# Optimization experiments

Hardware: AMD Instinct MI355X
Metric: run time of the kernel (lower is better)

Reference implementation:

```python
import jax, jax.numpy as jnp
import numpy as np

B = 8192      # batch (num nodes)
D = 256       # embedding dim
K = 8         # positives per node -> nnz = B*K
EPS = 1e-8


def setup_inputs() -> dict:
    key = jax.random.key(0)
    k_emb, k_val = jax.random.split(key)
    embeddings = jax.random.normal(k_emb, (B, D), dtype=jnp.float32)
    # structured sparse positive mask: node i is positive with (i+1..i+K) mod B
    # -> unique pairs, row-major sorted (coalesced), no self loops
    rows = jnp.repeat(jnp.arange(B, dtype=jnp.int64), K)           # [B*K]
    offs = jnp.tile(jnp.arange(1, K + 1, dtype=jnp.int64), B)      # [B*K]
    cols = (rows + offs) % B
    pos_vals = jax.random.uniform(k_val, (B * K,), dtype=jnp.float32)
    temperature = jnp.float32(0.5)  # learnable scalar nn.Parameter
    return {
        "embeddings": embeddings,
        "pos_vals": pos_vals,
        "temperature": temperature,
        "pos_row": rows,
        "pos_col": cols,
    }


def reference(embeddings, pos_vals, temperature, pos_row, pos_col):
    n = embeddings.shape[0]
    # F.normalize(p=2, dim=1) with eps=1e-12
    norm = jnp.linalg.norm(embeddings, axis=1, keepdims=True)
    z = embeddings / jnp.maximum(norm, 1e-12)

    temp = jax.nn.softplus(temperature)
    sim = jnp.matmul(z, z.T) / temp                                 # [B,B]
    sim = sim - jax.lax.stop_gradient(jnp.max(sim, axis=1, keepdims=True))

    pos_dense = jnp.zeros((n, n), dtype=bool).at[pos_row, pos_col].set(True)
    identity = jnp.eye(n, dtype=bool)
    neg_mask = (~pos_dense) & (~identity)

    # pos weights: 'inverse_sim' -> 1 - values, min-max normalized
    pos_w = 1.0 - pos_vals
    pos_w = (pos_w - jnp.min(pos_w)) / (jnp.max(pos_w) - jnp.min(pos_w) + EPS)

    # neg weights: 'inverse_sim' -> min-max over negative sims, +1; weight_mat=1 elsewhere
    neg_min = jnp.min(jnp.where(neg_mask, sim, jnp.inf))
    neg_max = jnp.max(jnp.where(neg_mask, sim, -jnp.inf))
    neg_w = (sim - neg_min) / (neg_max - neg_min + EPS) + 1.0
    log_weight = jnp.where(neg_mask, jnp.log(neg_w), 0.0)

    log_probs = sim - jax.nn.logsumexp(sim + log_weight, axis=1, keepdims=True)

    pos_log = log_probs[pos_row, pos_col]   # same ordering as torch boolean index (coalesced mask)
    loss = -jnp.mean(pos_log * pos_w)
    return loss
```

## Files before the change

kernel.cpp:

```cpp
#include <hip/hip_runtime.h>

#define NB 8192
#define ND 256
#define NMASK 8191
#define CEPS 1e-8f
#define L2E 1.4426950408889634f
#define LN2 0.6931471805599453f
#define SC1 0x7F7F7F7F

#if __has_builtin(__builtin_amdgcn_exp2f)
#define EXP2(x) __builtin_amdgcn_exp2f(x)
#else
#define EXP2(x) exp2f(x)
#endif

#define DPPF(x, ctrl) \
  __int_as_float(__builtin_amdgcn_update_dpp(0, __float_as_int(x), (ctrl), 0xF, 0xF, true))

__device__ __forceinline__ float sum16(float x) {
  x += DPPF(x, 0xB1);
  x += DPPF(x, 0x4E);
  x += DPPF(x, 0x124);
  x += DPPF(x, 0x128);
  return x;
}
__device__ __forceinline__ float min16(float x) {
  x = fminf(x, DPPF(x, 0xB1));
  x = fminf(x, DPPF(x, 0x4E));
  x = fminf(x, DPPF(x, 0x124));
  x = fminf(x, DPPF(x, 0x128));
  return x;
}
__device__ __forceinline__ float max16(float x) {
  x = fmaxf(x, DPPF(x, 0xB1));
  x = fmaxf(x, DPPF(x, 0x4E));
  x = fmaxf(x, DPPF(x, 0x124));
  x = fmaxf(x, DPPF(x, 0x128));
  return x;
}

typedef float f32x4 __attribute__((ext_vector_type(4)));
typedef float f32x2 __attribute__((ext_vector_type(2)));
typedef int v8i __attribute__((ext_vector_type(8)));
typedef int v4i __attribute__((ext_vector_type(4)));
union V8 { v8i v; v4i q[2]; };


__global__ void k_norm(const float* __restrict__ emb, const float* __restrict__ temperature,
                       const float* __restrict__ pos_vals, char* __restrict__ zb8,
                       float* __restrict__ EpF,
                       float* __restrict__ bpvmin, float* __restrict__ bpvmax,
                       float* __restrict__ out) {
  const int tid = threadIdx.x, lane = tid & 63, w = tid >> 6;
  const int bid = blockIdx.x;
  if (bid == 0 && tid == 0) out[0] = 0.f;
  float sp = log1pf(expf(temperature[0]));
  float alpha = sqrtf(L2E / sp);
  int row = bid * 4 + w;
  const float4 e = *(const float4*)(emb + row * ND + lane * 4);
  float ss = e.x * e.x + e.y * e.y + e.z * e.z + e.w * e.w;
#pragma unroll
  for (int mk = 1; mk < 64; mk <<= 1) ss += __shfl_xor(ss, mk, 64);
  float rn = alpha / fmaxf(sqrtf(ss), 1e-12f);
  int pk = __builtin_amdgcn_cvt_pk_fp8_f32(e.x * rn, e.y * rn, 0, 0);
  pk = __builtin_amdgcn_cvt_pk_fp8_f32(e.z * rn, e.w * rn, pk, 1);
  *(int*)(zb8 + row * 256 + lane * 4) = pk;
  if (lane < 2) EpF[row * 2 + lane] = 0.f;
  if (w == 0) {
    float v = (lane < 32) ? pos_vals[bid * 32 + lane] : 0.f;
    float mn = (lane < 32) ? v : INFINITY;
    float mx = (lane < 32) ? v : -INFINITY;
#pragma unroll
    for (int mk = 1; mk < 32; mk <<= 1) {
      mn = fminf(mn, __shfl_xor(mn, mk, 64));
      mx = fmaxf(mx, __shfl_xor(mx, mk, 64));
    }
    if (lane == 0) { bpvmin[bid] = mn; bpvmax[bid] = mx; }
  }
}

__global__ __launch_bounds__(256) void k_gemm(
    const char* __restrict__ zb8, float* __restrict__ EpF,
    float* __restrict__ sBand, float* __restrict__ bmin, float* __restrict__ bmax) {
  __shared__ __align__(16) char smem[32768];
  const int tid = threadIdx.x, lane = tid & 63, w = tid >> 6;
  const int l15 = lane & 15, lq = lane >> 4;
  const int bid = blockIdx.x;
  int d, rb;
  if (bid < 2048) { d = bid >> 6; rb = bid & 63; }
  else { d = 32; rb = bid - 2048; }
  const int cb = (rb + d) & 63;
  const int roww = rb * 128 + w * 32;
  const int colbase = cb * 128;

#pragma unroll
  for (int i = 0; i < 8; ++i) {
    int s = w * 8 + i, T = s >> 1, h = s & 1, ct = T >> 1, kc = T & 1;
    const char* g = zb8 + (colbase + ct * 16 + l15) * 256 + kc * 128 + lq * 32 + h * 16;
    __builtin_amdgcn_global_load_lds(
        (const __attribute__((address_space(1))) void*)(g),
        (__attribute__((address_space(3))) void*)(smem + s * 1024), 16, 0, 0);
  }

  V8 aF[2][2];
#pragma unroll
  for (int mt = 0; mt < 2; ++mt) {
    const char* ar = zb8 + (roww + mt * 16 + l15) * 256 + lq * 32;
#pragma unroll
    for (int kc = 0; kc < 2; ++kc) {
      aF[mt][kc].q[0] = *(const v4i*)(ar + kc * 128);
      aF[mt][kc].q[1] = *(const v4i*)(ar + kc * 128 + 16);
    }
  }

  f32x2 E1v[4], Eav[4];
#pragma unroll
  for (int i = 0; i < 4; ++i) { E1v[i] = (f32x2){0.f, 0.f}; Eav[i] = (f32x2){0.f, 0.f}; }
  float2 cA[4][2];
#pragma unroll
  for (int s = 0; s < 4; ++s) { cA[s][0] = make_float2(0.f, 0.f); cA[s][1] = make_float2(0.f, 0.f); }
  float vmn = INFINITY, vmx = -INFINITY;

  __syncthreads();

#pragma unroll
  for (int step = 0; step < 4; ++step) {
    f32x4 acc[2][2];
#pragma unroll
    for (int mt = 0; mt < 2; ++mt) {
      acc[mt][0] = (f32x4){0.f, 0.f, 0.f, 0.f};
      acc[mt][1] = (f32x4){0.f, 0.f, 0.f, 0.f};
    }
#pragma unroll
    for (int kc = 0; kc < 2; ++kc) {
      V8 b0, b1;
      const char* t0 = smem + ((step * 2 + 0) * 2 + kc) * 2048;
      const char* t1 = smem + ((step * 2 + 1) * 2 + kc) * 2048;
      b0.q[0] = *(const v4i*)(t0 + lane * 16);
      b0.q[1] = *(const v4i*)(t0 + 1024 + lane * 16);
      b1.q[0] = *(const v4i*)(t1 + lane * 16);
      b1.q[1] = *(const v4i*)(t1 + 1024 + lane * 16);
#pragma unroll
      for (int mt = 0; mt < 2; ++mt) {
        acc[mt][0] = __builtin_amdgcn_mfma_scale_f32_16x16x128_f8f6f4(
            aF[mt][kc].v, b0.v, acc[mt][0], 0, 0, 0, SC1, 0, SC1);
        acc[mt][1] = __builtin_amdgcn_mfma_scale_f32_16x16x128_f8f6f4(
            aF[mt][kc].v, b1.v, acc[mt][1], 0, 0, 0, SC1, 0, SC1);
      }
    }
    const int offbase = (colbase + step * 32 + l15) - (roww + lq * 4);
    if (d >= 2) {
#pragma unroll
      for (int mt = 0; mt < 2; ++mt)
#pragma unroll
        for (int nt = 0; nt < 2; ++nt) {
          f32x2 t01, t23, e01, e23;
          t01.x = acc[mt][nt][0]; t01.y = acc[mt][nt][1];
          t23.x = acc[mt][nt][2]; t23.y = acc[mt][nt][3];
          e01.x = EXP2(t01.x); e01.y = EXP2(t01.y);
          e23.x = EXP2(t23.x); e23.y = EXP2(t23.y);
          f32x2 m01 = e01 * t01, m23 = e23 * t23;
          E1v[mt * 2 + 0] += e01; E1v[mt * 2 + 1] += e23;
          Eav[mt * 2 + 0] += m01; Eav[mt * 2 + 1] += m23;
          f32x2 es = e01 + e23, ms = m01 + m23;
          cA[step][nt].x += es.x + es.y;
          cA[step][nt].y += ms.x + ms.y;
          vmn = fminf(fminf(t01.x, t01.y), vmn);
          vmn = fminf(fminf(t23.x, t23.y), vmn);
          vmx = fmaxf(fmaxf(t01.x, t01.y), vmx);
          vmx = fmaxf(fmaxf(t23.x, t23.y), vmx);
        }
    } else if (d == 1) {
#pragma unroll
      for (int mt = 0; mt < 2; ++mt)
#pragma unroll
        for (int nt = 0; nt < 2; ++nt)
#pragma unroll
          for (int reg = 0; reg < 4; ++reg) {
            float t = acc[mt][nt][reg];
            float e = EXP2(t);
            E1v[mt * 2 + (reg >> 1)][reg & 1] += e;
            Eav[mt * 2 + (reg >> 1)][reg & 1] = fmaf(e, t, Eav[mt * 2 + (reg >> 1)][reg & 1]);
            cA[step][nt].x += e;
            cA[step][nt].y = fmaf(e, t, cA[step][nt].y);
            vmn = fminf(vmn, t);
            vmx = fmaxf(vmx, t);
            int off = (offbase + (nt - mt) * 16 - reg) & NMASK;
            if (off <= 8)
              sBand[(roww + mt * 16 + lq * 4 + reg) * 16 + off] = t;
          }
    } else {
#pragma unroll
      for (int mt = 0; mt < 2; ++mt)
#pragma unroll
        for (int nt = 0; nt < 2; ++nt)
#pragma unroll
          for (int reg = 0; reg < 4; ++reg) {
            float t = acc[mt][nt][reg];
            float e = EXP2(t);
            E1v[mt * 2 + (reg >> 1)][reg & 1] += e;
            Eav[mt * 2 + (reg >> 1)][reg & 1] = fmaf(e, t, Eav[mt * 2 + (reg >> 1)][reg & 1]);
            int off = (offbase + (nt - mt) * 16 - reg) & NMASK;
            bool isB = off <= 8;
            vmn = fminf(vmn, isB ? vmn : t);
            vmx = fmaxf(vmx, isB ? vmx : t);
            if (isB)
              sBand[(roww + mt * 16 + lq * 4 + reg) * 16 + off] = t;
          }
    }
  }

#pragma unroll
  for (int i = 0; i < 4; ++i) {
    E1v[i].x = sum16(E1v[i].x); E1v[i].y = sum16(E1v[i].y);
    Eav[i].x = sum16(Eav[i].x); Eav[i].y = sum16(Eav[i].y);
  }
  if (l15 == 0) {
#pragma unroll
    for (int mt = 0; mt < 2; ++mt)
#pragma unroll
      for (int p = 0; p < 2; ++p) {
        int r0 = roww + mt * 16 + lq * 4 + p * 2;
        atomicAdd(&EpF[r0 * 2 + 0], E1v[mt * 2 + p].x);
        atomicAdd(&EpF[r0 * 2 + 1], Eav[mt * 2 + p].x);
        atomicAdd(&EpF[r0 * 2 + 2], E1v[mt * 2 + p].y);
        atomicAdd(&EpF[r0 * 2 + 3], Eav[mt * 2 + p].y);
      }
  }
  vmn = min16(vmn);
  vmx = max16(vmx);
  vmn = fminf(vmn, __shfl_xor(vmn, 16, 64));
  vmx = fmaxf(vmx, __shfl_xor(vmx, 16, 64));
  vmn = fminf(vmn, __shfl_xor(vmn, 32, 64));
  vmx = fmaxf(vmx, __shfl_xor(vmx, 32, 64));
  __syncthreads();
  float2* colAcc = (float2*)smem;
  float* redmm = (float*)(smem + 16384);
  if (d != 0) {
#pragma unroll
    for (int s = 0; s < 4; ++s)
#pragma unroll
      for (int nt = 0; nt < 2; ++nt)
        colAcc[(w * 4 + lq) * 128 + s * 32 + nt * 16 + l15] = cA[s][nt];
  }
  if (lane == 0) { redmm[w] = vmn; redmm[4 + w] = vmx; }
  __syncthreads();
  if (d != 0 && tid < 128) {
    float sx = 0.f, sy = 0.f;
#pragma unroll
    for (int j = 0; j < 16; ++j) {
      float2 p = colAcc[j * 128 + tid];
      sx += p.x;
      sy += p.y;
    }
    atomicAdd(&EpF[(colbase + tid) * 2 + 0], sx);
    atomicAdd(&EpF[(colbase + tid) * 2 + 1], sy);
  }
  if (tid == 0) {
    bmin[bid] = fminf(fminf(redmm[0], redmm[1]), fminf(redmm[2], redmm[3]));
    bmax[bid] = fmaxf(fmaxf(redmm[4], redmm[5]), fmaxf(redmm[6], redmm[7]));
  }
}

__global__ void k_final(const float* __restrict__ pos_vals, const float* __restrict__ EpF,
                        const float* __restrict__ sBand,
                        const float* __restrict__ bmin, const float* __restrict__ bmax,
                        const float* __restrict__ bpvmin, const float* __restrict__ bpvmax,
                        float* __restrict__ out) {
  const int tid = threadIdx.x, lane = tid & 63, w = tid >> 6;
  __shared__ float sv[16];
  __shared__ float coef[4];
  float mn = INFINITY, mx = -INFINITY, pmn = INFINITY, pmx = -INFINITY;
  for (int i = tid; i < 2080; i += 256) { mn = fminf(mn, bmin[i]); mx = fmaxf(mx, bmax[i]); }
  for (int i = tid; i < 2048; i += 256) { pmn = fminf(pmn, bpvmin[i]); pmx = fmaxf(pmx, bpvmax[i]); }
#pragma unroll
  for (int mk = 1; mk < 64; mk <<= 1) {
    mn = fminf(mn, __shfl_xor(mn, mk, 64));
    mx = fmaxf(mx, __shfl_xor(mx, mk, 64));
    pmn = fminf(pmn, __shfl_xor(pmn, mk, 64));
    pmx = fmaxf(pmx, __shfl_xor(pmx, mk, 64));
  }
  if (lane == 0) { sv[w] = mn; sv[4 + w] = mx; sv[8 + w] = pmn; sv[12 + w] = pmx; }
  __syncthreads();
  if (tid == 0) {
    float tmin = fminf(fminf(sv[0], sv[1]), fminf(sv[2], sv[3]));
    float tmax = fmaxf(fmaxf(sv[4], sv[5]), fmaxf(sv[6], sv[7]));
    float pvmin = fminf(fminf(sv[8], sv[9]), fminf(sv[10], sv[11]));
    float pvmax = fmaxf(fmaxf(sv[12], sv[13]), fmaxf(sv[14], sv[15]));
    float At = LN2 / ((tmax - tmin) * LN2 + CEPS);
    coef[0] = At;
    coef[1] = 1.f - At * tmin;
    coef[2] = pvmax;
    coef[3] = 1.f / (pvmax - pvmin + CEPS);
  }
  __syncthreads();
  const float At = coef[0], Bt = coef[1], pvmax = coef[2], pwInv = coef[3];

  const int row = blockIdx.x * 256 + tid;
  const float2 ep = *(const float2*)(EpF + row * 2);
  float e1 = ep.x, ea = ep.y;
  const float4* sb4 = (const float4*)(sBand + (size_t)row * 16);
  float4 b0 = sb4[0], b1 = sb4[1], b2 = sb4[2];
  float tb[9] = {b0.x, b0.y, b0.z, b0.w, b1.x, b1.y, b1.z, b1.w, b2.x};
  float Sb = 0.f, Sbt = 0.f;
#pragma unroll
  for (int o = 0; o <= 8; ++o) {
    float e = EXP2(tb[o]);
    Sb += e;
    Sbt = fmaf(e, tb[o], Sbt);
  }
  float denom = At * (ea - Sbt) + Bt * (e1 - Sb) + Sb;
  float lse = logf(denom);
  const float4* pv4 = (const float4*)(pos_vals + (size_t)row * 8);
  float4 pva = pv4[0], pvb = pv4[1];
  float pv[8] = {pva.x, pva.y, pva.z, pva.w, pvb.x, pvb.y, pvb.z, pvb.w};
  float contrib = 0.f;
#pragma unroll
  for (int k = 0; k < 8; ++k)
    contrib += (pvmax - pv[k]) * pwInv * (tb[k + 1] * LN2 - lse);
#pragma unroll
  for (int mk = 1; mk < 64; mk <<= 1) contrib += __shfl_xor(contrib, mk, 64);
  __syncthreads();
  if (lane == 0) sv[w] = contrib;
  __syncthreads();
  if (tid == 0)
    atomicAdd(out, -(sv[0] + sv[1] + sv[2] + sv[3]) * (1.0f / 65536.0f));
}

extern "C" void kernel_launch(void* const* d_in, const int* in_sizes, int n_in,
                              void* d_out, int out_size, void* d_ws, size_t ws_size,
                              hipStream_t stream) {
  const float* emb = (const float*)d_in[0];
  const float* pos_vals = (const float*)d_in[1];
  const float* temperature = (const float*)d_in[2];
  float* out = (float*)d_out;

  char* ws = (char*)d_ws;
  size_t off = 0;
  float* EpF = (float*)(ws + off); off += (size_t)NB * 2 * 4;
  float* sBand = (float*)(ws + off); off += (size_t)NB * 16 * 4;
  float* bmin = (float*)(ws + off); off += 2080 * 4 + 128;
  float* bmax = (float*)(ws + off); off += 2080 * 4 + 128;
  float* bpvmin = (float*)(ws + off); off += 2048 * 4;
  float* bpvmax = (float*)(ws + off); off += 2048 * 4;
  char* zb8 = (char*)(ws + off); off += (size_t)NB * 256;

  k_norm<<<2048, 256, 0, stream>>>(emb, temperature, pos_vals, zb8, EpF, bpvmin, bpvmax, out);
  k_gemm<<<2080, 256, 0, stream>>>(zb8, EpF, sBand, bmin, bmax);
  k_final<<<32, 256, 0, stream>>>(pos_vals, EpF, sBand, bmin, bmax, bpvmin, bpvmax, out);
}
```

Before: 101.0 us.

## Fuse norm, GEMM and final passes into one cooperative persistent kernel

```diff
diff --git a/kernel.cpp b/kernel.cpp
--- a/kernel.cpp
+++ b/kernel.cpp
@@ -1,4 +1,7 @@
 #include <hip/hip_runtime.h>
+#include <hip/hip_cooperative_groups.h>
+
+namespace cg = cooperative_groups;
 
 #define NB 8192
 #define ND 256
@@ -7,6 +10,7 @@
 #define L2E 1.4426950408889634f
 #define LN2 0.6931471805599453f
 #define SC1 0x7F7F7F7F
+#define NTILE 2080
 
 #if __has_builtin(__builtin_amdgcn_exp2f)
 #define EXP2(x) __builtin_amdgcn_exp2f(x)
@@ -45,6 +49,303 @@
 typedef int v4i __attribute__((ext_vector_type(4)));
 union V8 { v8i v; v4i q[2]; };
 
+
+__global__ __launch_bounds__(256) void k_all(
+    const float* __restrict__ emb, const float* __restrict__ pos_vals,
+    const float* __restrict__ temperature, char* __restrict__ zb8,
+    float* __restrict__ EpF, float* __restrict__ sBand,
+    float* __restrict__ bmin, float* __restrict__ bmax,
+    float* __restrict__ bpvmin, float* __restrict__ bpvmax,
+    float* __restrict__ out) {
+  __shared__ __align__(16) char smem[32768];
+  const int tid = threadIdx.x, lane = tid & 63, w = tid >> 6;
+  const int l15 = lane & 15, lq = lane >> 4;
+  const int bid = blockIdx.x, g = gridDim.x;
+  const int gtid = bid * 256 + tid, nth = g * 256;
+  cg::grid_group grid = cg::this_grid();
+
+  {
+    float sp = log1pf(expf(temperature[0]));
+    float alpha = sqrtf(L2E / sp);
+    const int nwave = g * 4, gw = bid * 4 + w;
+    for (int row = gw; row < NB; row += nwave) {
+      const float4 e = *(const float4*)(emb + row * ND + lane * 4);
+      float ss = e.x * e.x + e.y * e.y + e.z * e.z + e.w * e.w;
+#pragma unroll
+      for (int mk = 1; mk < 64; mk <<= 1) ss += __shfl_xor(ss, mk, 64);
+      float rn = alpha / fmaxf(sqrtf(ss), 1e-12f);
+      int pk = __builtin_amdgcn_cvt_pk_fp8_f32(e.x * rn, e.y * rn, 0, 0);
+      pk = __builtin_amdgcn_cvt_pk_fp8_f32(e.z * rn, e.w * rn, pk, 1);
+      *(int*)(zb8 + row * 256 + lane * 4) = pk;
+    }
+    for (int i = gtid; i < NB * 2; i += nth) EpF[i] = 0.f;
+    if (gtid == 0) out[0] = 0.f;
+    float pmn = INFINITY, pmx = -INFINITY;
+    for (int i = gtid; i < NB * 8; i += nth) {
+      float v = pos_vals[i];
+      pmn = fminf(pmn, v);
+      pmx = fmaxf(pmx, v);
+    }
+#pragma unroll
+    for (int mk = 1; mk < 64; mk <<= 1) {
+      pmn = fminf(pmn, __shfl_xor(pmn, mk, 64));
+      pmx = fmaxf(pmx, __shfl_xor(pmx, mk, 64));
+    }
+    float* s0 = (float*)smem;
+    if (lane == 0) { s0[w] = pmn; s0[4 + w] = pmx; }
+    __syncthreads();
+    if (tid == 0) {
+      bpvmin[bid] = fminf(fminf(s0[0], s0[1]), fminf(s0[2], s0[3]));
+      bpvmax[bid] = fmaxf(fmaxf(s0[4], s0[5]), fmaxf(s0[6], s0[7]));
+    }
+  }
+  __threadfence();
+  grid.sync();
+
+  float vmn = INFINITY, vmx = -INFINITY;
+  for (int tile = bid; tile < NTILE; tile += g) {
+    int d, rb;
+    if (tile < 2048) { d = tile >> 6; rb = tile & 63; }
+    else { d = 32; rb = tile - 2048; }
+    const int cb = (rb + d) & 63;
+    const int roww = rb * 128 + w * 32;
+    const int colbase = cb * 128;
+
+    __syncthreads();
+#pragma unroll
+    for (int i = 0; i < 8; ++i) {
+      int s = w * 8 + i, T = s >> 1, h = s & 1, ct = T >> 1, kc = T & 1;
+      const char* gp = zb8 + (colbase + ct * 16 + l15) * 256 + kc * 128 + lq * 32 + h * 16;
+      __builtin_amdgcn_global_load_lds(
+          (const __attribute__((address_space(1))) void*)(gp),
+          (__attribute__((address_space(3))) void*)(smem + s * 1024), 16, 0, 0);
+    }
+    V8 aF[2][2];
+#pragma unroll
+    for (int mt = 0; mt < 2; ++mt) {
+      const char* ar = zb8 + (roww + mt * 16 + l15) * 256 + lq * 32;
+#pragma unroll
+      for (int kc = 0; kc < 2; ++kc) {
+        aF[mt][kc].q[0] = *(const v4i*)(ar + kc * 128);
+        aF[mt][kc].q[1] = *(const v4i*)(ar + kc * 128 + 16);
+      }
+    }
+    f32x2 E1v[4], Eav[4];
+#pragma unroll
+    for (int i = 0; i < 4; ++i) { E1v[i] = (f32x2){0.f, 0.f}; Eav[i] = (f32x2){0.f, 0.f}; }
+    float2 cA[4][2];
+#pragma unroll
+    for (int s = 0; s < 4; ++s) { cA[s][0] = make_float2(0.f, 0.f); cA[s][1] = make_float2(0.f, 0.f); }
+
+    __syncthreads();
+
+#pragma unroll
+    for (int step = 0; step < 4; ++step) {
+      f32x4 acc[2][2];
+#pragma unroll
+      for (int mt = 0; mt < 2; ++mt) {
+        acc[mt][0] = (f32x4){0.f, 0.f, 0.f, 0.f};
+        acc[mt][1] = (f32x4){0.f, 0.f, 0.f, 0.f};
+      }
+#pragma unroll
+      for (int kc = 0; kc < 2; ++kc) {
+        V8 b0, b1;
+        const char* t0 = smem + ((step * 2 + 0) * 2 + kc) * 2048;
+        const char* t1 = smem + ((step * 2 + 1) * 2 + kc) * 2048;
+        b0.q[0] = *(const v4i*)(t0 + lane * 16);
+        b0.q[1] = *(const v4i*)(t0 + 1024 + lane * 16);
+        b1.q[0] = *(const v4i*)(t1 + lane * 16);
+        b1.q[1] = *(const v4i*)(t1 + 1024 + lane * 16);
+#pragma unroll
+        for (int mt = 0; mt < 2; ++mt) {
+          acc[mt][0] = __builtin_amdgcn_mfma_scale_f32_16x16x128_f8f6f4(
+              aF[mt][kc].v, b0.v, acc[mt][0], 0, 0, 0, SC1, 0, SC1);
+          acc[mt][1] = __builtin_amdgcn_mfma_scale_f32_16x16x128_f8f6f4(
+              aF[mt][kc].v, b1.v, acc[mt][1], 0, 0, 0, SC1, 0, SC1);
+        }
+      }
+      const int offbase = (colbase + step * 32 + l15) - (roww + lq * 4);
+      if (d >= 2) {
+#pragma unroll
+        for (int mt = 0; mt < 2; ++mt)
+#pragma unroll
+          for (int nt = 0; nt < 2; ++nt) {
+            f32x2 t01, t23, e01, e23;
+            t01.x = acc[mt][nt][0]; t01.y = acc[mt][nt][1];
+            t23.x = acc[mt][nt][2]; t23.y = acc[mt][nt][3];
+            e01.x = EXP2(t01.x); e01.y = EXP2(t01.y);
+            e23.x = EXP2(t23.x); e23.y = EXP2(t23.y);
+            f32x2 m01 = e01 * t01, m23 = e23 * t23;
+            E1v[mt * 2 + 0] += e01; E1v[mt * 2 + 1] += e23;
+            Eav[mt * 2 + 0] += m01; Eav[mt * 2 + 1] += m23;
+            f32x2 es = e01 + e23, ms = m01 + m23;
+            cA[step][nt].x += es.x + es.y;
+            cA[step][nt].y += ms.x + ms.y;
+            vmn = fminf(fminf(t01.x, t01.y), vmn);
+            vmn = fminf(fminf(t23.x, t23.y), vmn);
+            vmx = fmaxf(fmaxf(t01.x, t01.y), vmx);
+            vmx = fmaxf(fmaxf(t23.x, t23.y), vmx);
+          }
+      } else if (d == 1) {
+#pragma unroll
+        for (int mt = 0; mt < 2; ++mt)
+#pragma unroll
+          for (int nt = 0; nt < 2; ++nt)
+#pragma unroll
+            for (int reg = 0; reg < 4; ++reg) {
+              float t = acc[mt][nt][reg];
+              float e = EXP2(t);
+              E1v[mt * 2 + (reg >> 1)][reg & 1] += e;
+              Eav[mt * 2 + (reg >> 1)][reg & 1] = fmaf(e, t, Eav[mt * 2 + (reg >> 1)][reg & 1]);
+              cA[step][nt].x += e;
+              cA[step][nt].y = fmaf(e, t, cA[step][nt].y);
+              vmn = fminf(vmn, t);
+              vmx = fmaxf(vmx, t);
+              int off = (offbase + (nt - mt) * 16 - reg) & NMASK;
+              if (off <= 8)
+                sBand[(roww + mt * 16 + lq * 4 + reg) * 16 + off] = t;
+            }
+      } else {
+#pragma unroll
+        for (int mt = 0; mt < 2; ++mt)
+#pragma unroll
+          for (int nt = 0; nt < 2; ++nt)
+#pragma unroll
+            for (int reg = 0; reg < 4; ++reg) {
+              float t = acc[mt][nt][reg];
+              float e = EXP2(t);
+              E1v[mt * 2 + (reg >> 1)][reg & 1] += e;
+              Eav[mt * 2 + (reg >> 1)][reg & 1] = fmaf(e, t, Eav[mt * 2 + (reg >> 1)][reg & 1]);
+              int off = (offbase + (nt - mt) * 16 - reg) & NMASK;
+              bool isB = off <= 8;
+              vmn = fminf(vmn, isB ? vmn : t);
+              vmx = fmaxf(vmx, isB ? vmx : t);
+              if (isB)
+                sBand[(roww + mt * 16 + lq * 4 + reg) * 16 + off] = t;
+            }
+      }
+    }
+
+#pragma unroll
+    for (int i = 0; i < 4; ++i) {
+      E1v[i].x = sum16(E1v[i].x); E1v[i].y = sum16(E1v[i].y);
+      Eav[i].x = sum16(Eav[i].x); Eav[i].y = sum16(Eav[i].y);
+    }
+    if (l15 == 0) {
+#pragma unroll
+      for (int mt = 0; mt < 2; ++mt)
+#pragma unroll
+        for (int p = 0; p < 2; ++p) {
+          int r0 = roww + mt * 16 + lq * 4 + p * 2;
+          atomicAdd(&EpF[r0 * 2 + 0], E1v[mt * 2 + p].x);
+          atomicAdd(&EpF[r0 * 2 + 1], Eav[mt * 2 + p].x);
+          atomicAdd(&EpF[r0 * 2 + 2], E1v[mt * 2 + p].y);
+          atomicAdd(&EpF[r0 * 2 + 3], Eav[mt * 2 + p].y);
+        }
+    }
+    __syncthreads();
+    float2* colAcc = (float2*)smem;
+    if (d != 0) {
+#pragma unroll
+      for (int s = 0; s < 4; ++s)
+#pragma unroll
+        for (int nt = 0; nt < 2; ++nt)
+          colAcc[(w * 4 + lq) * 128 + s * 32 + nt * 16 + l15] = cA[s][nt];
+    }
+    __syncthreads();
+    if (d != 0 && tid < 128) {
+      float sx = 0.f, sy = 0.f;
+#pragma unroll
+      for (int j = 0; j < 16; ++j) {
+        float2 p = colAcc[j * 128 + tid];
+        sx += p.x;
+        sy += p.y;
+      }
+      atomicAdd(&EpF[(colbase + tid) * 2 + 0], sx);
+      atomicAdd(&EpF[(colbase + tid) * 2 + 1], sy);
+    }
+  }
+  vmn = min16(vmn);
+  vmx = max16(vmx);
+  vmn = fminf(vmn, __shfl_xor(vmn, 16, 64));
+  vmx = fmaxf(vmx, __shfl_xor(vmx, 16, 64));
+  vmn = fminf(vmn, __shfl_xor(vmn, 32, 64));
+  vmx = fmaxf(vmx, __shfl_xor(vmx, 32, 64));
+  __syncthreads();
+  float* redmm = (float*)(smem + 16384);
+  if (lane == 0) { redmm[w] = vmn; redmm[4 + w] = vmx; }
+  __syncthreads();
+  if (tid == 0) {
+    bmin[bid] = fminf(fminf(redmm[0], redmm[1]), fminf(redmm[2], redmm[3]));
+    bmax[bid] = fmaxf(fmaxf(redmm[4], redmm[5]), fmaxf(redmm[6], redmm[7]));
+  }
+  __threadfence();
+  grid.sync();
+
+  if (bid >= NB / 256) return;
+  float* sv = (float*)smem;
+  float* coef = (float*)(smem + 64);
+  {
+    float mn = INFINITY, mx = -INFINITY, pmn = INFINITY, pmx = -INFINITY;
+    for (int i = tid; i < g; i += 256) {
+      mn = fminf(mn, bmin[i]); mx = fmaxf(mx, bmax[i]);
+      pmn = fminf(pmn, bpvmin[i]); pmx = fmaxf(pmx, bpvmax[i]);
+    }
+#pragma unroll
+    for (int mk = 1; mk < 64; mk <<= 1) {
+      mn = fminf(mn, __shfl_xor(mn, mk, 64));
+      mx = fmaxf(mx, __shfl_xor(mx, mk, 64));
+      pmn = fminf(pmn, __shfl_xor(pmn, mk, 64));
+      pmx = fmaxf(pmx, __shfl_xor(pmx, mk, 64));
+    }
+    __syncthreads();
+    if (lane == 0) { sv[w] = mn; sv[4 + w] = mx; sv[8 + w] = pmn; sv[12 + w] = pmx; }
+    __syncthreads();
+    if (tid == 0) {
+      float tmin = fminf(fminf(sv[0], sv[1]), fminf(sv[2], sv[3]));
+      float tmax = fmaxf(fmaxf(sv[4], sv[5]), fmaxf(sv[6], sv[7]));
+      float pvmin = fminf(fminf(sv[8], sv[9]), fminf(sv[10], sv[11]));
+      float pvmax = fmaxf(fmaxf(sv[12], sv[13]), fmaxf(sv[14], sv[15]));
+      float At = LN2 / ((tmax - tmin) * LN2 + CEPS);
+      coef[0] = At;
+      coef[1] = 1.f - At * tmin;
+      coef[2] = pvmax;
+      coef[3] = 1.f / (pvmax - pvmin + CEPS);
+    }
+    __syncthreads();
+  }
+  const float At = coef[0], Bt = coef[1], pvmax = coef[2], pwInv = coef[3];
+
+  const int row = gtid;
+  const float2 ep = *(const float2*)(EpF + row * 2);
+  float e1 = ep.x, ea = ep.y;
+  const float4* sb4 = (const float4*)(sBand + (size_t)row * 16);
+  float4 b0 = sb4[0], b1 = sb4[1], b2 = sb4[2];
+  float tb[9] = {b0.x, b0.y, b0.z, b0.w, b1.x, b1.y, b1.z, b1.w, b2.x};
+  float Sb = 0.f, Sbt = 0.f;
+#pragma unroll
+  for (int o = 0; o <= 8; ++o) {
+    float e = EXP2(tb[o]);
+    Sb += e;
+    Sbt = fmaf(e, tb[o], Sbt);
+  }
+  float denom = At * (ea - Sbt) + Bt * (e1 - Sb) + Sb;
+  float lse = logf(denom);
+  const float4* pv4 = (const float4*)(pos_vals + (size_t)row * 8);
+  float4 pva = pv4[0], pvb = pv4[1];
+  float pv[8] = {pva.x, pva.y, pva.z, pva.w, pvb.x, pvb.y, pvb.z, pvb.w};
+  float contrib = 0.f;
+#pragma unroll
+  for (int k = 0; k < 8; ++k)
+    contrib += (pvmax - pv[k]) * pwInv * (tb[k + 1] * LN2 - lse);
+#pragma unroll
+  for (int mk = 1; mk < 64; mk <<= 1) contrib += __shfl_xor(contrib, mk, 64);
+  __syncthreads();
+  if (lane == 0) sv[w] = contrib;
+  __syncthreads();
+  if (tid == 0)
+    atomicAdd(out, -(sv[0] + sv[1] + sv[2] + sv[3]) * (1.0f / 65536.0f));
+}
 
 __global__ void k_norm(const float* __restrict__ emb, const float* __restrict__ temperature,
                        const float* __restrict__ pos_vals, char* __restrict__ zb8,
@@ -92,16 +393,14 @@
   const int cb = (rb + d) & 63;
   const int roww = rb * 128 + w * 32;
   const int colbase = cb * 128;
-
 #pragma unroll
   for (int i = 0; i < 8; ++i) {
     int s = w * 8 + i, T = s >> 1, h = s & 1, ct = T >> 1, kc = T & 1;
-    const char* g = zb8 + (colbase + ct * 16 + l15) * 256 + kc * 128 + lq * 32 + h * 16;
+    const char* gp = zb8 + (colbase + ct * 16 + l15) * 256 + kc * 128 + lq * 32 + h * 16;
     __builtin_amdgcn_global_load_lds(
-        (const __attribute__((address_space(1))) void*)(g),
+        (const __attribute__((address_space(1))) void*)(gp),
         (__attribute__((address_space(3))) void*)(smem + s * 1024), 16, 0, 0);
   }
-
   V8 aF[2][2];
 #pragma unroll
   for (int mt = 0; mt < 2; ++mt) {
@@ -112,7 +411,6 @@
       aF[mt][kc].q[1] = *(const v4i*)(ar + kc * 128 + 16);
     }
   }
-
   f32x2 E1v[4], Eav[4];
 #pragma unroll
   for (int i = 0; i < 4; ++i) { E1v[i] = (f32x2){0.f, 0.f}; Eav[i] = (f32x2){0.f, 0.f}; }
@@ -120,9 +418,7 @@
 #pragma unroll
   for (int s = 0; s < 4; ++s) { cA[s][0] = make_float2(0.f, 0.f); cA[s][1] = make_float2(0.f, 0.f); }
   float vmn = INFINITY, vmx = -INFINITY;
-
-  __syncthreads();
-
+  __syncthreads();
 #pragma unroll
   for (int step = 0; step < 4; ++step) {
     f32x4 acc[2][2];
@@ -209,7 +505,6 @@
           }
     }
   }
-
 #pragma unroll
   for (int i = 0; i < 4; ++i) {
     E1v[i].x = sum16(E1v[i].x); E1v[i].y = sum16(E1v[i].y);
@@ -295,7 +590,6 @@
   }
   __syncthreads();
   const float At = coef[0], Bt = coef[1], pvmax = coef[2], pwInv = coef[3];
-
   const int row = blockIdx.x * 256 + tid;
   const float2 ep = *(const float2*)(EpF + row * 2);
   float e1 = ep.x, ea = ep.y;
@@ -339,13 +633,36 @@
   size_t off = 0;
   float* EpF = (float*)(ws + off); off += (size_t)NB * 2 * 4;
   float* sBand = (float*)(ws + off); off += (size_t)NB * 16 * 4;
-  float* bmin = (float*)(ws + off); off += 2080 * 4 + 128;
-  float* bmax = (float*)(ws + off); off += 2080 * 4 + 128;
-  float* bpvmin = (float*)(ws + off); off += 2048 * 4;
-  float* bpvmax = (float*)(ws + off); off += 2048 * 4;
+  float* bmin = (float*)(ws + off); off += 4096 * 4;
+  float* bmax = (float*)(ws + off); off += 4096 * 4;
+  float* bpvmin = (float*)(ws + off); off += 4096 * 4;
+  float* bpvmax = (float*)(ws + off); off += 4096 * 4;
   char* zb8 = (char*)(ws + off); off += (size_t)NB * 256;
 
-  k_norm<<<2048, 256, 0, stream>>>(emb, temperature, pos_vals, zb8, EpF, bpvmin, bpvmax, out);
-  k_gemm<<<2080, 256, 0, stream>>>(zb8, EpF, sBand, bmin, bmax);
-  k_final<<<32, 256, 0, stream>>>(pos_vals, EpF, sBand, bmin, bmax, bpvmin, bpvmax, out);
-}
+  static int gridSize = -2;
+  if (gridSize == -2) {
+    int r = 0;
+    if (hipOccupancyMaxActiveBlocksPerMultiprocessor(&r, k_all, 256, 0) == hipSuccess && r > 0) {
+      long gsz = (long)r * 256;
+      gridSize = (int)(gsz > 1024 ? 1024 : gsz);
+    } else {
+      gridSize = -1;
+    }
+  }
+  bool done = false;
+  if (gridSize > 0) {
+    void* args[] = {(void*)&emb, (void*)&pos_vals, (void*)&temperature, (void*)&zb8,
+                    (void*)&EpF, (void*)&sBand, (void*)&bmin, (void*)&bmax,
+                    (void*)&bpvmin, (void*)&bpvmax, (void*)&out};
+    if (hipLaunchCooperativeKernel(k_all, dim3(gridSize), dim3(256), args, 0, stream) ==
+        hipSuccess)
+      done = true;
+    else
+      gridSize = -1;
+  }
+  if (!done) {
+    k_norm<<<2048, 256, 0, stream>>>(emb, temperature, pos_vals, zb8, EpF, bpvmin, bpvmax, out);
+    k_gemm<<<2080, 256, 0, stream>>>(zb8, EpF, sBand, bmin, bmax);
+    k_final<<<32, 256, 0, stream>>>(pos_vals, EpF, sBand, bmin, bmax, bpvmin, bpvmax, out);
+  }
+}
```

Result: slower. 208.3 us (+106.3%).
